# Kernel tuning notes

Measured on AMD Instinct MI355X. Metric: run time of the kernel, lower is better.

The kernel has to match this reference:

```python
import jax, jax.numpy as jnp
import numpy as np

B, S, D = 2, 2048, 768
H = 12
DEPTH = D // H
DFF = 4 * D
EPS = 1e-5


def setup_inputs() -> dict:
    key = jax.random.key(0)
    ks = jax.random.split(key, 9)
    sd = 0.02
    return {
        "x": jax.random.normal(ks[0], (B, S, D), dtype=jnp.float32),
        "Wqkv": jax.random.normal(ks[1], (D, 3 * D), dtype=jnp.float32) * sd,
        "Wout": jax.random.normal(ks[2], (D, D), dtype=jnp.float32) * sd,
        "bout": jnp.zeros((D,), dtype=jnp.float32),
        "W1": jax.random.normal(ks[3], (D, DFF), dtype=jnp.float32) * sd,
        "b1": jnp.zeros((DFF,), dtype=jnp.float32),
        "W2": jax.random.normal(ks[4], (DFF, D), dtype=jnp.float32) * sd,
        "b2": jnp.zeros((D,), dtype=jnp.float32),
        "g1": jnp.ones((D,), dtype=jnp.float32),
        "be1": jnp.zeros((D,), dtype=jnp.float32),
        "g2": jnp.ones((D,), dtype=jnp.float32),
        "be2": jnp.zeros((D,), dtype=jnp.float32),
    }


def _layernorm(x, gain, bias):
    mean = jnp.mean(x, axis=-1, keepdims=True)
    var = jnp.mean(jnp.square(x - mean), axis=-1, keepdims=True)  # unbiased=False
    return gain * (x - mean) / jnp.sqrt(var + EPS) + bias


def reference(x, Wqkv, Wout, bout, W1, b1, W2, b2, g1, be1, g2, be2):
    b, s, d = x.shape
    # QKV projection (no bias), chunk into q,k,v
    qkv = jnp.einsum("bsd,de->bse", x, Wqkv)
    q, k, v = jnp.split(qkv, 3, axis=-1)
    q = q.reshape(b, s, H, DEPTH).transpose(0, 2, 1, 3)  # bhsd
    k = k.reshape(b, s, H, DEPTH).transpose(0, 2, 1, 3)
    v = v.reshape(b, s, H, DEPTH).transpose(0, 2, 1, 3)
    scores = jnp.einsum("bhqd,bhkd->bhqk", q, k) / np.sqrt(DEPTH).astype(np.float32)
    # causal mask (use_masking=True)
    causal = jnp.tril(jnp.ones((s, s), dtype=bool))
    scores = jnp.where(causal, scores, -jnp.inf)
    attn = jax.nn.softmax(scores, axis=-1)
    ctx = jnp.einsum("bhqk,bhkd->bhqd", attn, v)
    ctx = ctx.transpose(0, 2, 1, 3).reshape(b, s, d)
    attn_out = jnp.einsum("bsd,de->bse", ctx, Wout) + bout
    # residual + LN1 (dropout is identity in eval)
    h = _layernorm(x + attn_out, g1, be1)
    # FFN
    ff = jax.nn.relu(jnp.einsum("bsd,df->bsf", h, W1) + b1)
    ff = jnp.einsum("bsf,fd->bsd", ff, W2) + b2
    return _layernorm(h + ff, g2, be2)
```

## Files before the change

### kernel.cpp

```cpp
#include <hip/hip_runtime.h>


typedef __attribute__((ext_vector_type(8)))  short    short8;
typedef __attribute__((ext_vector_type(4)))  float    floatx4;
typedef __attribute__((ext_vector_type(16))) float    floatx16;
typedef __attribute__((ext_vector_type(4)))  unsigned uint4v;

#define QSC 0.18033688f
#define C2  24.0f

__device__ __forceinline__ float b2f(unsigned short u) {
    return __uint_as_float(((unsigned)u) << 16);
}
__device__ __forceinline__ unsigned short f2b(float f) {
    unsigned x = __float_as_uint(f);
    return (unsigned short)((x + 0x7fffu + ((x >> 16) & 1u)) >> 16);
}
__device__ __forceinline__ void async_cp16(const void* g, void* l) {
    __builtin_amdgcn_global_load_lds((const __attribute__((address_space(1))) void*)g,
                                     (__attribute__((address_space(3))) void*)l,
                                     16, 0, 0);
}
__device__ __forceinline__ unsigned cvtpk(float lo, float hi) {
    unsigned r;
    asm("v_cvt_pk_bf16_f32 %0, %1, %2" : "=v"(r) : "v"(lo), "v"(hi));
    return r;
}
__device__ __forceinline__ void plswap(unsigned& a, unsigned& b) {
    asm("v_permlane32_swap_b32 %0, %1" : "+v"(a), "+v"(b));
}
__device__ __forceinline__ int chunk_ofs8(int qb) {
    int t = qb >> 2, rem = qb & 3;
    return (t + 1) * (2 * t + rem);
}
__device__ __forceinline__ int swz16(int row, int chunk) {
    return row * 64 + (((chunk ^ (row & 7)) & 7) << 3);
}
__device__ __forceinline__ int swzB(int row, int chunk) {
    return row * 64 + (((chunk ^ (row & 7) ^ ((row >> 2) & 6)) & 7) << 3);
}

__global__ __launch_bounds__(256) void prep_all(
    const float* __restrict__ x,    unsigned short* __restrict__ xb,
    const float* __restrict__ Wqkv, unsigned short* __restrict__ wqkvT,
    const float* __restrict__ Wout, unsigned short* __restrict__ woutT,
    const float* __restrict__ W1,   unsigned short* __restrict__ w1T,
    const float* __restrict__ W2,   unsigned short* __restrict__ w2T)
{
    __shared__ float tile[32][33];
    int idx = blockIdx.x;
    int tx = threadIdx.x & 31, ty = threadIdx.x >> 5;
    if (idx >= 6912) {
        int i = (idx - 6912) * 256 + threadIdx.x;
        float4 v = ((const float4*)x)[i];
        ushort4 u;
        u.x = f2b(v.x); u.y = f2b(v.y); u.z = f2b(v.z); u.w = f2b(v.w);
        ((ushort4*)xb)[i] = u;
        return;
    }
    const float* W; unsigned short* Wt; int K, N, bx, by;
    if (idx < 1728)      { W = Wqkv; Wt = wqkvT; K = 768;  N = 2304; bx = idx % 72;        by = idx / 72; }
    else if (idx < 2304) { W = Wout; Wt = woutT; K = 768;  N = 768;  bx = (idx-1728) % 24; by = (idx-1728) / 24; }
    else if (idx < 4608) { W = W1;   Wt = w1T;   K = 768;  N = 3072; bx = (idx-2304) % 96; by = (idx-2304) / 96; }
    else                 { W = W2;   Wt = w2T;   K = 3072; N = 768;  bx = (idx-4608) % 24; by = (idx-4608) / 24; }
    int n0 = bx * 32, k0 = by * 32;
    for (int i = ty; i < 32; i += 8)
        tile[i][tx] = W[(size_t)(k0 + i) * N + n0 + tx];
    __syncthreads();
    for (int i = ty; i < 32; i += 8)
        Wt[(size_t)(n0 + i) * K + k0 + tx] = f2b(tile[tx][i]);
}

__global__ __launch_bounds__(256) void gemm_bf16(
    const unsigned short* __restrict__ A,
    const unsigned short* __restrict__ Bt,
    const float* __restrict__ bias,
    float* __restrict__ outF,
    unsigned short* __restrict__ outB,
    int M, int N, int K, int relu, int mode, int kslab)
{
    __shared__ unsigned short As[2][8192];
    __shared__ unsigned short Bs[2][8192];
    const int tid  = threadIdx.x;
    const int gx   = gridDim.x;
    const int nwg  = gx * gridDim.y;
    const int orig = blockIdx.y * gx + blockIdx.x;
    const int qch  = nwg >> 3, rem = nwg & 7;
    const int xcd  = orig & 7, sub = orig >> 3;
    const int nid  = (xcd < rem ? xcd * (qch + 1)
                                : rem * (qch + 1) + (xcd - rem) * qch) + sub;
    const int m0   = (nid / gx) * 128;
    const int n0   = (nid % gx) * 128;
    const int kz   = blockIdx.z;
    const int kbeg = kz * kslab;
    const int kend = kbeg + kslab;
    const int lane = tid & 63;
    const int wave = tid >> 6;
    const int wm   = (wave >> 1) * 64;
    const int wn   = (wave & 1) * 64;
    const int fr   = lane & 15;
    const int fq   = lane >> 4;

    floatx4 acc[4][4];
    for (int i = 0; i < 4; i++)
        for (int j = 0; j < 4; j++)
            for (int e = 0; e < 4; e++) acc[i][j][e] = 0.f;

#define STAGE(BUF, KK)                                                         \
    {                                                                          \
        _Pragma("unroll")                                                      \
        for (int r_ = 0; r_ < 4; ++r_) {                                       \
            int c_   = r_ * 256 + tid;       \
            int row_ = c_ >> 3;                                                \
            int jj_  = ((c_ & 7) ^ (row_ & 7)) * 8;  \
            async_cp16(A  + (size_t)(m0 + row_) * K + (KK) + jj_, &As[BUF][c_ * 8]); \
            async_cp16(Bt + (size_t)(n0 + row_) * K + (KK) + jj_, &Bs[BUF][c_ * 8]); \
        }                                                                      \
    }

    STAGE(0, kbeg);
    asm volatile("s_waitcnt vmcnt(0)" ::: "memory");
    __builtin_amdgcn_s_barrier();
    int cur = 0;
    for (int kk = kbeg; kk < kend; kk += 64) {
        const bool more = (kk + 64 < kend);
        if (more) {
            STAGE(cur ^ 1, kk + 64);
            asm volatile("s_waitcnt vmcnt(8)" ::: "memory");
        } else {
            asm volatile("s_waitcnt vmcnt(0)" ::: "memory");
        }
        __builtin_amdgcn_s_barrier();
        #pragma unroll
        for (int kc = 0; kc < 2; ++kc) {
            short8 a[4], b[4];
            #pragma unroll
            for (int t = 0; t < 4; t++) a[t] = *(const short8*)&As[cur][swz16(wm + t * 16 + fr, kc * 4 + fq)];
            #pragma unroll
            for (int t = 0; t < 4; t++) b[t] = *(const short8*)&Bs[cur][swz16(wn + t * 16 + fr, kc * 4 + fq)];
            #pragma unroll
            for (int i = 0; i < 4; i++)
                #pragma unroll
                for (int j = 0; j < 4; j++)
                    acc[i][j] = __builtin_amdgcn_mfma_f32_16x16x32_bf16(a[i], b[j], acc[i][j], 0, 0, 0);
        }
        asm volatile("s_waitcnt lgkmcnt(0)" ::: "memory");
        __builtin_amdgcn_s_barrier();
        cur ^= 1;
    }
#undef STAGE

    if (mode == 1) {
        #pragma unroll
        for (int j = 0; j < 4; j++) {
            int col   = n0 + wn + j * 16 + fr;
            int which = (col >= 1536) ? 2 : (col >= 768 ? 1 : 0);
            float sc  = (which == 0) ? QSC : 1.0f;
            int rem_  = col - which * 768;
            int hh    = rem_ >> 6, d = rem_ & 63;
            #pragma unroll
            for (int i = 0; i < 4; i++) {
                int rbase = m0 + wm + i * 16 + fq * 4;
                #pragma unroll
                for (int e = 0; e < 4; e++) {
                    int row = rbase + e;
                    int b_  = row >> 11, srow = row & 2047;
                    size_t idx = (size_t)which * 3145728 +
                                 ((size_t)(b_ * 12 + hh) * 2048 + srow) * 64 + d;
                    outB[idx] = f2b(acc[i][j][e] * sc);
                }
            }
        }
        return;
    }
    #pragma unroll
    for (int j = 0; j < 4; j++) {
        int col  = n0 + wn + j * 16 + fr;
        float bv = bias ? bias[col] : 0.f;
        #pragma unroll
        for (int i = 0; i < 4; i++) {
            int rbase = m0 + wm + i * 16 + fq * 4;
            #pragma unroll
            for (int e = 0; e < 4; e++) {
                float v = acc[i][j][e] + bv;
                if (relu) v = fmaxf(v, 0.f);
                size_t idx = (size_t)(rbase + e) * N + col;
                if (outF) outF[idx] = v;
                if (outB) outB[idx] = f2b(v);
            }
        }
    }
}

__global__ __launch_bounds__(256) void gemm_n64(
    const unsigned short* __restrict__ A,
    const unsigned short* __restrict__ Bt,
    float* __restrict__ outF,
    int K)
{
    __shared__ unsigned short As[2][8192];
    __shared__ unsigned short Bs[2][4096];
    const int tid  = threadIdx.x;
    const int nwg  = 384;
    const int orig = blockIdx.y * 12 + blockIdx.x;
    const int qch  = nwg >> 3;
    const int nid  = (orig & 7) * qch + (orig >> 3);
    const int m0   = (nid / 12) * 128;
    const int n0   = (nid % 12) * 64;
    const int lane = tid & 63;
    const int wave = tid >> 6;
    const int wm   = wave * 32;
    const int fr   = lane & 15;
    const int fq   = lane >> 4;

    floatx4 acc[2][4];
    for (int i = 0; i < 2; i++)
        for (int j = 0; j < 4; j++)
            for (int e = 0; e < 4; e++) acc[i][j][e] = 0.f;

#define STAGE64(BUF, KK)                                                       \
    {                                                                          \
        _Pragma("unroll")                                                      \
        for (int r_ = 0; r_ < 4; ++r_) {                                       \
            int c_   = r_ * 256 + tid;                                         \
            int row_ = c_ >> 3;                                                \
            int jj_  = ((c_ & 7) ^ (row_ & 7)) * 8;                            \
            async_cp16(A + (size_t)(m0 + row_) * K + (KK) + jj_, &As[BUF][c_ * 8]); \
        }                                                                      \
        _Pragma("unroll")                                                      \
        for (int r_ = 0; r_ < 2; ++r_) {                                       \
            int c_   = r_ * 256 + tid;           \
            int row_ = c_ >> 3;                                                \
            int jj_  = ((c_ & 7) ^ (row_ & 7)) * 8;                            \
            async_cp16(Bt + (size_t)(n0 + row_) * K + (KK) + jj_, &Bs[BUF][c_ * 8]); \
        }                                                                      \
    }

    STAGE64(0, 0);
    asm volatile("s_waitcnt vmcnt(0)" ::: "memory");
    __builtin_amdgcn_s_barrier();
    int cur = 0;
    for (int kk = 0; kk < K; kk += 64) {
        const bool more = (kk + 64 < K);
        if (more) {
            STAGE64(cur ^ 1, kk + 64);
            asm volatile("s_waitcnt vmcnt(6)" ::: "memory");
        } else {
            asm volatile("s_waitcnt vmcnt(0)" ::: "memory");
        }
        __builtin_amdgcn_s_barrier();
        #pragma unroll
        for (int kc = 0; kc < 2; ++kc) {
            short8 a[2], b[4];
            #pragma unroll
            for (int t = 0; t < 2; t++) a[t] = *(const short8*)&As[cur][swz16(wm + t * 16 + fr, kc * 4 + fq)];
            #pragma unroll
            for (int t = 0; t < 4; t++) b[t] = *(const short8*)&Bs[cur][swz16(t * 16 + fr, kc * 4 + fq)];
            #pragma unroll
            for (int i = 0; i < 2; i++)
                #pragma unroll
                for (int j = 0; j < 4; j++)
                    acc[i][j] = __builtin_amdgcn_mfma_f32_16x16x32_bf16(a[i], b[j], acc[i][j], 0, 0, 0);
        }
        asm volatile("s_waitcnt lgkmcnt(0)" ::: "memory");
        __builtin_amdgcn_s_barrier();
        cur ^= 1;
    }
#undef STAGE64

    #pragma unroll
    for (int j = 0; j < 4; j++) {
        int col = n0 + j * 16 + fr;
        #pragma unroll
        for (int i = 0; i < 2; i++) {
            int rbase = m0 + wm + i * 16 + fq * 4;
            #pragma unroll
            for (int e = 0; e < 4; e++)
                outF[(size_t)(rbase + e) * 768 + col] = acc[i][j][e];
        }
    }
}

__global__ __launch_bounds__(256) void attn_part(const unsigned short* __restrict__ Qg,
                                                 const unsigned short* __restrict__ Kg,
                                                 const unsigned short* __restrict__ Vg,
                                                 unsigned short* __restrict__ pO,
                                                 float* __restrict__ pL) {
    __shared__ unsigned short Ks[2][4096];
    __shared__ unsigned short Vt[2][4096];
    const int tid  = threadIdx.x;
    const int lane = tid & 63;
    const int wave = tid >> 6;
    const int ql   = lane & 31;
    const int hi   = lane >> 5;
    const int wm   = wave * 32;
    const int bid  = blockIdx.y * 40 + blockIdx.x;
    const int swz  = (bid & 7) * 120 + (bid >> 3);
    const int bh   = swz / 40;
    const int r    = 39 - (swz % 40);
    int qb = 0;
    for (int q_ = 15; q_ >= 0; --q_) if (r >= chunk_ofs8(q_)) { qb = q_; break; }
    const int c     = r - chunk_ofs8(qb);
    const int q0    = qb * 128;
    const int tile0 = 8 * c;
    const int ntk   = min(8, 2 * (qb + 1) - 8 * c);
    const int slot  = bh * 40 + r;
    const unsigned short* Qb = Qg + (size_t)bh * 131072;
    const unsigned short* Kb = Kg + (size_t)bh * 131072;
    const unsigned short* Vb = Vg + (size_t)bh * 131072;
    const int qrow = q0 + wm + ql;

    short8 qf[4];
    {
        const unsigned short* qr = Qb + (size_t)qrow * 64 + hi * 8;
        #pragma unroll
        for (int c4 = 0; c4 < 4; ++c4)
            qf[c4] = *(const short8*)(qr + c4 * 16);
    }

    floatx16 o[2];
    #pragma unroll
    for (int db = 0; db < 2; ++db)
        #pragma unroll
        for (int e = 0; e < 16; ++e) o[db][e] = 0.f;
    float ls[4] = {0.f, 0.f, 0.f, 0.f};

    const int c0 = tid, c1 = tid + 256;
    uint4 vr0, vr1;

#define KSTAGE(BUF, TG)                                                        \
    {                                                                          \
        int base_ = (TG) * 64;                                                 \
        int r0_ = c0 >> 3, j0_ = (c0 & 7) ^ (r0_ & 7) ^ ((r0_ >> 2) & 6);      \
        int r1_ = c1 >> 3, j1_ = (c1 & 7) ^ (r1_ & 7) ^ ((r1_ >> 2) & 6);      \
        async_cp16(Kb + (size_t)(base_ + r0_) * 64 + (j0_ & 7) * 8,            \
                   &Ks[BUF][c0 * 8]);                                          \
        async_cp16(Kb + (size_t)(base_ + r1_) * 64 + (j1_ & 7) * 8,            \
                   &Ks[BUF][c1 * 8]);                                          \
    }
#define LOADV(TG)                                                              \
    {                                                                          \
        int base = (TG) * 64;                                                  \
        vr0 = *(const uint4*)(Vb + (size_t)(base + (c0 & 63)) * 64 + (c0 >> 6) * 8); \
        vr1 = *(const uint4*)(Vb + (size_t)(base + (c1 & 63)) * 64 + (c1 >> 6) * 8); \
    }
#define WRITEV(BUF)                                                            \
    {                                                                          \
        unsigned short t0[8]; *(uint4*)t0 = vr0;                               \
        _Pragma("unroll") for (int i_ = 0; i_ < 8; ++i_) {                     \
            int rv = (c0 >> 6) * 8 + i_;                                       \
            Vt[BUF][rv * 64 + (((((c0 >> 3) & 7) ^ i_ ^ ((rv >> 2) & 6)) & 7) << 3) + (c0 & 7)] = t0[i_]; \
        }                                                                      \
        unsigned short t1[8]; *(uint4*)t1 = vr1;                               \
        _Pragma("unroll") for (int i_ = 0; i_ < 8; ++i_) {                     \
            int rv = (c1 >> 6) * 8 + i_;                                       \
            Vt[BUF][rv * 64 + (((((c1 >> 3) & 7) ^ i_ ^ ((rv >> 2) & 6)) & 7) << 3) + (c1 & 7)] = t1[i_]; \
        }                                                                      \
    }

    KSTAGE(0, tile0);
    LOADV(tile0);
    WRITEV(0);
    __syncthreads();

    for (int kt = 0; kt < ntk; ++kt) {
        const int  tg   = tile0 + kt;
        const int  cur  = kt & 1;
        const bool more = (kt + 1 < ntk);
        if (more) {
            KSTAGE(cur ^ 1, tg + 1);
            LOADV(tg + 1);
        }

        #pragma unroll
        for (int bb = 0; bb < 2; ++bb) {
            short8 kf[4];
            #pragma unroll
            for (int c4 = 0; c4 < 4; ++c4)
                kf[c4] = *(const short8*)&Ks[cur][swzB(32 * bb + ql, 2 * c4 + hi)];
            floatx16 s;
            #pragma unroll
            for (int e = 0; e < 16; ++e) s[e] = 0.f;
            #pragma unroll
            for (int c4 = 0; c4 < 4; ++c4)
                s = __builtin_amdgcn_mfma_f32_32x32x16_bf16(kf[c4], qf[c4], s, 0, 0, 0);

            const int  kvb = tg * 64 + 32 * bb + 4 * hi;
            const bool nm  = (tg * 64 + 32 * bb + 31) > (q0 + wm);
            if (nm) {
                #pragma unroll
                for (int e = 0; e < 16; ++e)
                    if (kvb + (e & 3) + 8 * (e >> 2) > qrow) s[e] = -1e30f;
            }
            float pv[16];
            #pragma unroll
            for (int e = 0; e < 16; ++e) {
                pv[e] = __builtin_amdgcn_exp2f(s[e] - C2);
                ls[e & 3] += pv[e];
            }

            unsigned w[8];
            #pragma unroll
            for (int m = 0; m < 4; ++m) {
                w[2 * m]     = cvtpk(pv[4 * m],     pv[4 * m + 1]);
                w[2 * m + 1] = cvtpk(pv[4 * m + 2], pv[4 * m + 3]);
            }
            plswap(w[0], w[2]);
            plswap(w[1], w[3]);
            plswap(w[4], w[6]);
            plswap(w[5], w[7]);
            uint4v u0 = {w[0], w[1], w[2], w[3]};
            uint4v u1 = {w[4], w[5], w[6], w[7]};
            short8 pa0 = __builtin_bit_cast(short8, u0);
            short8 pa1 = __builtin_bit_cast(short8, u1);

            #pragma unroll
            for (int db = 0; db < 2; ++db) {
                short8 vf0 = *(const short8*)&Vt[cur][swzB(32 * db + ql, 4 * bb + hi)];
                short8 vf1 = *(const short8*)&Vt[cur][swzB(32 * db + ql, 4 * bb + 2 + hi)];
                o[db] = __builtin_amdgcn_mfma_f32_32x32x16_bf16(pa0, vf0, o[db], 0, 0, 0);
                o[db] = __builtin_amdgcn_mfma_f32_32x32x16_bf16(pa1, vf1, o[db], 0, 0, 0);
            }
        }

        if (more) {
            WRITEV(cur ^ 1);
            __syncthreads();
        }
    }
#undef KSTAGE
#undef LOADV
#undef WRITEV

    float lsum = (ls[0] + ls[1]) + (ls[2] + ls[3]);
    lsum += __shfl_xor(lsum, 32);
    if (lane < 32)
        pL[(size_t)slot * 128 + wm + ql] = lsum;

    __syncthreads();
    unsigned short* Ost = &Ks[0][0];
    #pragma unroll
    for (int db = 0; db < 2; ++db)
        #pragma unroll
        for (int e = 0; e < 16; ++e) {
            int row = wm + (e & 3) + 8 * (e >> 2) + 4 * hi;
            int col = db * 32 + ql;
            Ost[row * 64 + ((((col >> 3) ^ (row & 7)) & 7) << 3) + (col & 7)] =
                f2b(o[db][e]);
        }
    __syncthreads();
    #pragma unroll
    for (int p = 0; p < 4; ++p) {
        int chunk = p * 256 + tid;
        int row = chunk >> 3, cc = chunk & 7;
        uint4 val = *(const uint4*)&Ost[row * 64 + (((cc ^ (row & 7)) & 7) << 3)];
        *(uint4*)(pO + ((size_t)slot * 128 + row) * 64 + cc * 8) = val;
    }
}

__global__ __launch_bounds__(256) void attn_combine(const unsigned short* __restrict__ pO,
                                                    const float* __restrict__ pL,
                                                    unsigned short* __restrict__ ctx) {
    const int qb  = blockIdx.x;
    const int bh  = blockIdx.y;
    const int b   = bh / 12, h = bh % 12;
    const int nch = (qb >> 2) + 1;
    const int slot0 = bh * 40 + chunk_ofs8(qb);
    const int tid = threadIdx.x;
    const int row = tid >> 1;
    const int col0 = (tid & 1) * 32;

    float L = 0.f;
    for (int i = 0; i < nch; ++i)
        L += pL[(size_t)(slot0 + i) * 128 + row];

    float acc[32];
    #pragma unroll
    for (int j = 0; j < 32; ++j) acc[j] = 0.f;
    for (int i = 0; i < nch; ++i) {
        const unsigned short* p = pO + ((size_t)(slot0 + i) * 128 + row) * 64 + col0;
        #pragma unroll
        for (int v4 = 0; v4 < 4; ++v4) {
            uint4 u = *(const uint4*)(p + v4 * 8);
            unsigned short t[8]; *(uint4*)t = u;
            #pragma unroll
            for (int j = 0; j < 8; ++j) acc[v4 * 8 + j] += b2f(t[j]);
        }
    }
    float inv = 1.f / L;
    unsigned short* orow = ctx + ((size_t)(b * 2048 + qb * 128 + row)) * 768 + h * 64 + col0;
    #pragma unroll
    for (int v4 = 0; v4 < 4; ++v4) {
        unsigned short t[8];
        #pragma unroll
        for (int j = 0; j < 8; ++j) t[j] = f2b(acc[v4 * 8 + j] * inv);
        *(uint4*)(orow + v4 * 8) = *(uint4*)t;
    }
}

__global__ __launch_bounds__(256) void resid_ln2(const float* __restrict__ X,
                                                 const float* __restrict__ P,
                                                 int nsplit,
                                                 const float* __restrict__ bv,
                                                 const float* __restrict__ gain,
                                                 const float* __restrict__ beta,
                                                 float* __restrict__ outF,
                                                 unsigned short* __restrict__ outB) {
    const int row = blockIdx.x;
    const int t   = threadIdx.x;
    const size_t off = (size_t)row * 768;
    float v[3];
    #pragma unroll
    for (int i = 0; i < 3; i++) {
        size_t c = off + t + i * 256;
        float r = X[c] + bv[t + i * 256];
        for (int p = 0; p < nsplit; ++p) r += P[(size_t)p * 3145728 + c];
        v[i] = r;
    }
    float s  = v[0] + v[1] + v[2];
    float s2 = v[0] * v[0] + v[1] * v[1] + v[2] * v[2];
    #pragma unroll
    for (int o2 = 32; o2 > 0; o2 >>= 1) {
        s  += __shfl_down(s,  o2);
        s2 += __shfl_down(s2, o2);
    }
    __shared__ float rs[4], rq[4];
    if ((t & 63) == 0) { rs[t >> 6] = s; rq[t >> 6] = s2; }
    __syncthreads();
    float S    = rs[0] + rs[1] + rs[2] + rs[3];
    float S2   = rq[0] + rq[1] + rq[2] + rq[3];
    float mean = S * (1.0f / 768.0f);
    float var  = S2 * (1.0f / 768.0f) - mean * mean;
    float inv  = rsqrtf(var + 1e-5f);
    #pragma unroll
    for (int i = 0; i < 3; i++) {
        int c   = t + i * 256;
        float y = gain[c] * (v[i] - mean) * inv + beta[c];
        if (outF) outF[off + c] = y;
        if (outB) outB[off + c] = f2b(y);
    }
}

extern "C" void kernel_launch(void* const* d_in, const int* in_sizes, int n_in,
                              void* d_out, int out_size, void* d_ws, size_t ws_size,
                              hipStream_t stream) {
    const float* x    = (const float*)d_in[0];
    const float* Wqkv = (const float*)d_in[1];
    const float* Wout = (const float*)d_in[2];
    const float* bout = (const float*)d_in[3];
    const float* W1   = (const float*)d_in[4];
    const float* b1   = (const float*)d_in[5];
    const float* W2   = (const float*)d_in[6];
    const float* b2   = (const float*)d_in[7];
    const float* g1   = (const float*)d_in[8];
    const float* be1  = (const float*)d_in[9];
    const float* g2   = (const float*)d_in[10];
    const float* be2  = (const float*)d_in[11];
    float* out = (float*)d_out;

    char* ws = (char*)d_ws;
    unsigned short* wqkvT  = (unsigned short*)(ws + 0);
    unsigned short* woutT  = (unsigned short*)(ws + 3538944);
    unsigned short* w1T    = (unsigned short*)(ws + 4718592);
    unsigned short* w2T    = (unsigned short*)(ws + 9437184);
    unsigned short* xb     = (unsigned short*)(ws + 14155776);
    unsigned short* qkvG   = (unsigned short*)(ws + 20447232);
    unsigned short* Qg     = qkvG;
    unsigned short* Kg     = qkvG + 3145728;
    unsigned short* Vg     = qkvG + 6291456;
    unsigned short* pO     = (unsigned short*)(ws + 39321600);
    float*          pL     = (float*)(ws + 67633152);
    unsigned short* ctxb   = (unsigned short*)(ws + 14155776);
    float*          WoutP  = (float*)(ws + 39321600);
    float*          h      = (float*)(ws + 20447232);
    unsigned short* hb     = (unsigned short*)(ws + 77070336);
    unsigned short* ffb    = (unsigned short*)(ws + 39321600);
    float*          W2P    = (float*)(ws + 64487424);

    prep_all<<<9984, 256, 0, stream>>>(x, xb, Wqkv, wqkvT, Wout, woutT, W1, w1T, W2, w2T);
    gemm_bf16<<<dim3(18, 32), 256, 0, stream>>>(xb, wqkvT, nullptr, nullptr, qkvG,
                                                4096, 2304, 768, 0, 1, 768);
    attn_part<<<dim3(40, 24), 256, 0, stream>>>(Qg, Kg, Vg, pO, pL);
    attn_combine<<<dim3(16, 24), 256, 0, stream>>>(pO, pL, ctxb);
    gemm_n64<<<dim3(12, 32), 256, 0, stream>>>(ctxb, woutT, WoutP, 768);
    resid_ln2<<<4096, 256, 0, stream>>>(x, WoutP, 1, bout, g1, be1, h, hb);
    gemm_bf16<<<dim3(24, 32), 256, 0, stream>>>(hb, w1T, b1, nullptr, ffb,
                                                4096, 3072, 768, 1, 0, 768);
    gemm_n64<<<dim3(12, 32), 256, 0, stream>>>(ffb, w2T, W2P, 3072);
    resid_ln2<<<4096, 256, 0, stream>>>(h, W2P, 1, b2, g2, be2, out, nullptr);
}
```

Before: 296.9 us.

## Replace 128x128 GEMM with 256x256 eight-wave tile and phased prefetch pipeline

The QKV and FFN1 GEMMs move from a 128x128 tile with 256 threads to a 256x256 tile with 512 threads and 128 KB of double-buffered LDS. The main loop is split into phases that interleave async global-to-LDS copies of the next K slab with MFMA work, and each MFMA burst is bracketed by barriers and s_setprio. The larger tile raises operand reuse per LDS load and halves global traffic per FLOP. The cost is far fewer workgroups (144 and 192 on a 256-CU part), which risks leaving CUs idle, plus heavy register and LDS pressure.

```diff
diff --git a/kernel.cpp b/kernel.cpp
--- a/kernel.cpp
+++ b/kernel.cpp
@@ -71,122 +71,152 @@
         Wt[(size_t)(n0 + i) * K + k0 + tx] = f2b(tile[tx][i]);
 }
 
-__global__ __launch_bounds__(256) void gemm_bf16(
+__global__ __launch_bounds__(512) void gemm256(
     const unsigned short* __restrict__ A,
     const unsigned short* __restrict__ Bt,
     const float* __restrict__ bias,
-    float* __restrict__ outF,
     unsigned short* __restrict__ outB,
-    int M, int N, int K, int relu, int mode, int kslab)
+    int N, int K, int relu, int mode)
 {
-    __shared__ unsigned short As[2][8192];
-    __shared__ unsigned short Bs[2][8192];
+    __shared__ unsigned short L[2][4][8192];
     const int tid  = threadIdx.x;
     const int gx   = gridDim.x;
     const int nwg  = gx * gridDim.y;
     const int orig = blockIdx.y * gx + blockIdx.x;
-    const int qch  = nwg >> 3, rem = nwg & 7;
-    const int xcd  = orig & 7, sub = orig >> 3;
-    const int nid  = (xcd < rem ? xcd * (qch + 1)
-                                : rem * (qch + 1) + (xcd - rem) * qch) + sub;
-    const int m0   = (nid / gx) * 128;
-    const int n0   = (nid % gx) * 128;
-    const int kz   = blockIdx.z;
-    const int kbeg = kz * kslab;
-    const int kend = kbeg + kslab;
+    const int qch  = nwg >> 3;
+    const int nid  = (orig & 7) * qch + (orig >> 3);
+    const int m0   = (nid / gx) * 256;
+    const int n0   = (nid % gx) * 256;
     const int lane = tid & 63;
     const int wave = tid >> 6;
-    const int wm   = (wave >> 1) * 64;
-    const int wn   = (wave & 1) * 64;
+    const int wr   = wave >> 2;
+    const int wc   = wave & 3;
     const int fr   = lane & 15;
     const int fq   = lane >> 4;
-
-    floatx4 acc[4][4];
-    for (int i = 0; i < 4; i++)
+    const int bpart = 2 + (wc >> 1);
+    const int brow0 = (wc & 1) * 64;
+
+    floatx4 acc[8][4];
+    #pragma unroll
+    for (int i = 0; i < 8; i++)
+        #pragma unroll
         for (int j = 0; j < 4; j++)
+            #pragma unroll
             for (int e = 0; e < 4; e++) acc[i][j][e] = 0.f;
 
-#define STAGE(BUF, KK)                                                         \
+#define STGP(BUF, PART, GROW0, BASE, KK)                                       \
     {                                                                          \
         _Pragma("unroll")                                                      \
-        for (int r_ = 0; r_ < 4; ++r_) {                                       \
-            int c_   = r_ * 256 + tid;       \
+        for (int q_ = 0; q_ < 2; ++q_) {                                       \
+            int c_   = q_ * 512 + tid;                                         \
             int row_ = c_ >> 3;                                                \
-            int jj_  = ((c_ & 7) ^ (row_ & 7)) * 8;  \
-            async_cp16(A  + (size_t)(m0 + row_) * K + (KK) + jj_, &As[BUF][c_ * 8]); \
-            async_cp16(Bt + (size_t)(n0 + row_) * K + (KK) + jj_, &Bs[BUF][c_ * 8]); \
+            int jj_  = ((c_ & 7) ^ (row_ & 7)) * 8;                            \
+            async_cp16(BASE + (size_t)((GROW0) + row_) * K + (KK) + jj_,       \
+                       &L[BUF][PART][c_ * 8]);                                 \
         }                                                                      \
     }
 
-    STAGE(0, kbeg);
+#define PHASE(KT, MP)                                                          \
+    {                                                                          \
+        if ((MP) == 0) {                                                       \
+            _Pragma("unroll")                                                  \
+            for (int nj = 0; nj < 4; ++nj) {                                   \
+                bfr[nj][0] = *(const short8*)&L[KT][bpart][swz16(brow0 + nj * 16 + fr, fq)];     \
+                bfr[nj][1] = *(const short8*)&L[KT][bpart][swz16(brow0 + nj * 16 + fr, 4 + fq)]; \
+            }                                                                  \
+        }                                                                      \
+        short8 afr[2][2];                                                      \
+        _Pragma("unroll")                                                      \
+        for (int mm = 0; mm < 2; ++mm) {                                       \
+            afr[mm][0] = *(const short8*)&L[KT][wr][swz16(((MP) * 2 + mm) * 16 + fr, fq)];     \
+            afr[mm][1] = *(const short8*)&L[KT][wr][swz16(((MP) * 2 + mm) * 16 + fr, 4 + fq)]; \
+        }                                                                      \
+        __builtin_amdgcn_s_barrier();                                          \
+        asm volatile("s_waitcnt lgkmcnt(0)" ::: "memory");                     \
+        __builtin_amdgcn_sched_barrier(0);                                     \
+        __builtin_amdgcn_s_setprio(1);                                         \
+        _Pragma("unroll")                                                      \
+        for (int kc = 0; kc < 2; ++kc)                                         \
+            _Pragma("unroll")                                                  \
+            for (int mm = 0; mm < 2; ++mm)                                     \
+                _Pragma("unroll")                                              \
+                for (int nj = 0; nj < 4; ++nj)                                 \
+                    acc[(MP) * 2 + mm][nj] = __builtin_amdgcn_mfma_f32_16x16x32_bf16( \
+                        afr[mm][kc], bfr[nj][kc], acc[(MP) * 2 + mm][nj], 0, 0, 0);   \
+        __builtin_amdgcn_s_setprio(0);                                         \
+        __builtin_amdgcn_s_barrier();                                          \
+    }
+
+    short8 bfr[4][2];
+    const int niter = K >> 7;
+
+    STGP(0, 0, m0,       A,  0)
+    STGP(0, 1, m0 + 128, A,  0)
+    STGP(0, 2, n0,       Bt, 0)
+    STGP(0, 3, n0 + 128, Bt, 0)
     asm volatile("s_waitcnt vmcnt(0)" ::: "memory");
     __builtin_amdgcn_s_barrier();
-    int cur = 0;
-    for (int kk = kbeg; kk < kend; kk += 64) {
-        const bool more = (kk + 64 < kend);
-        if (more) {
-            STAGE(cur ^ 1, kk + 64);
-            asm volatile("s_waitcnt vmcnt(8)" ::: "memory");
-        } else {
-            asm volatile("s_waitcnt vmcnt(0)" ::: "memory");
-        }
-        __builtin_amdgcn_s_barrier();
-        #pragma unroll
-        for (int kc = 0; kc < 2; ++kc) {
-            short8 a[4], b[4];
-            #pragma unroll
-            for (int t = 0; t < 4; t++) a[t] = *(const short8*)&As[cur][swz16(wm + t * 16 + fr, kc * 4 + fq)];
-            #pragma unroll
-            for (int t = 0; t < 4; t++) b[t] = *(const short8*)&Bs[cur][swz16(wn + t * 16 + fr, kc * 4 + fq)];
-            #pragma unroll
-            for (int i = 0; i < 4; i++)
+
+    for (int it = 0; it < niter; ++it) {
+        const int k0   = it << 7;
+        const int k1   = k0 + 64;
+        const int kn   = k0 + 128;
+        const bool more = (it + 1 < niter);
+
+        STGP(1, 0, m0,       A,  k1)
+        STGP(1, 1, m0 + 128, A,  k1)
+        PHASE(0, 0)
+        STGP(1, 2, n0,       Bt, k1)
+        STGP(1, 3, n0 + 128, Bt, k1)
+        PHASE(0, 1)
+        PHASE(0, 2)
+        asm volatile("s_waitcnt vmcnt(0)" ::: "memory");
+        PHASE(0, 3)
+        if (more) { STGP(0, 0, m0, A, kn) STGP(0, 1, m0 + 128, A, kn) }
+        PHASE(1, 0)
+        if (more) { STGP(0, 2, n0, Bt, kn) STGP(0, 3, n0 + 128, Bt, kn) }
+        PHASE(1, 1)
+        PHASE(1, 2)
+        if (more) asm volatile("s_waitcnt vmcnt(0)" ::: "memory");
+        PHASE(1, 3)
+    }
+#undef STGP
+#undef PHASE
+
+    if (mode == 1) {
+        const int cb    = n0 + wc * 64;
+        const int which = (cb >= 1536) ? 2 : (cb >= 768 ? 1 : 0);
+        const int hh    = (cb - which * 768) >> 6;
+        const float sc  = (which == 0) ? QSC : 1.0f;
+        #pragma unroll
+        for (int mi = 0; mi < 8; ++mi) {
+            #pragma unroll
+            for (int nj = 0; nj < 4; ++nj) {
+                int d = nj * 16 + fr;
                 #pragma unroll
-                for (int j = 0; j < 4; j++)
-                    acc[i][j] = __builtin_amdgcn_mfma_f32_16x16x32_bf16(a[i], b[j], acc[i][j], 0, 0, 0);
-        }
-        asm volatile("s_waitcnt lgkmcnt(0)" ::: "memory");
-        __builtin_amdgcn_s_barrier();
-        cur ^= 1;
-    }
-#undef STAGE
-
-    if (mode == 1) {
-        #pragma unroll
-        for (int j = 0; j < 4; j++) {
-            int col   = n0 + wn + j * 16 + fr;
-            int which = (col >= 1536) ? 2 : (col >= 768 ? 1 : 0);
-            float sc  = (which == 0) ? QSC : 1.0f;
-            int rem_  = col - which * 768;
-            int hh    = rem_ >> 6, d = rem_ & 63;
-            #pragma unroll
-            for (int i = 0; i < 4; i++) {
-                int rbase = m0 + wm + i * 16 + fq * 4;
-                #pragma unroll
-                for (int e = 0; e < 4; e++) {
-                    int row = rbase + e;
-                    int b_  = row >> 11, srow = row & 2047;
+                for (int e = 0; e < 4; ++e) {
+                    int row  = m0 + wr * 128 + mi * 16 + fq * 4 + e;
+                    int b_   = row >> 11, srow = row & 2047;
                     size_t idx = (size_t)which * 3145728 +
                                  ((size_t)(b_ * 12 + hh) * 2048 + srow) * 64 + d;
-                    outB[idx] = f2b(acc[i][j][e] * sc);
+                    outB[idx] = f2b(acc[mi][nj][e] * sc);
                 }
             }
         }
         return;
     }
     #pragma unroll
-    for (int j = 0; j < 4; j++) {
-        int col  = n0 + wn + j * 16 + fr;
+    for (int nj = 0; nj < 4; ++nj) {
+        int col  = n0 + wc * 64 + nj * 16 + fr;
         float bv = bias ? bias[col] : 0.f;
         #pragma unroll
-        for (int i = 0; i < 4; i++) {
-            int rbase = m0 + wm + i * 16 + fq * 4;
-            #pragma unroll
-            for (int e = 0; e < 4; e++) {
-                float v = acc[i][j][e] + bv;
+        for (int mi = 0; mi < 8; ++mi) {
+            #pragma unroll
+            for (int e = 0; e < 4; ++e) {
+                int row = m0 + wr * 128 + mi * 16 + fq * 4 + e;
+                float v = acc[mi][nj][e] + bv;
                 if (relu) v = fmaxf(v, 0.f);
-                size_t idx = (size_t)(rbase + e) * N + col;
-                if (outF) outF[idx] = v;
-                if (outB) outB[idx] = f2b(v);
+                outB[(size_t)row * N + col] = f2b(v);
             }
         }
     }
@@ -578,14 +608,12 @@
     float*          W2P    = (float*)(ws + 64487424);
 
     prep_all<<<9984, 256, 0, stream>>>(x, xb, Wqkv, wqkvT, Wout, woutT, W1, w1T, W2, w2T);
-    gemm_bf16<<<dim3(18, 32), 256, 0, stream>>>(xb, wqkvT, nullptr, nullptr, qkvG,
-                                                4096, 2304, 768, 0, 1, 768);
+    gemm256<<<dim3(9, 16), 512, 0, stream>>>(xb, wqkvT, nullptr, qkvG, 2304, 768, 0, 1);
     attn_part<<<dim3(40, 24), 256, 0, stream>>>(Qg, Kg, Vg, pO, pL);
     attn_combine<<<dim3(16, 24), 256, 0, stream>>>(pO, pL, ctxb);
     gemm_n64<<<dim3(12, 32), 256, 0, stream>>>(ctxb, woutT, WoutP, 768);
     resid_ln2<<<4096, 256, 0, stream>>>(x, WoutP, 1, bout, g1, be1, h, hb);
-    gemm_bf16<<<dim3(24, 32), 256, 0, stream>>>(hb, w1T, b1, nullptr, ffb,
-                                                4096, 3072, 768, 1, 0, 768);
+    gemm256<<<dim3(12, 16), 512, 0, stream>>>(hb, w1T, b1, ffb, 3072, 768, 1, 0);
     gemm_n64<<<dim3(12, 32), 256, 0, stream>>>(ffb, w2T, W2P, 3072);
-    resid_ln2<<<4096, 256, 0, stream>>>(h, W2P, 1, b2, g2, be2, out, nullptr);
-}
+    resid_ln2<<<4096, 256, 0, stream>>>(h, W2P, 2 - 1, b2, g2, be2, out, nullptr);
+}
```

Result: faster. 285.2 us (-3.9%).
